# Kernel tuning notes

Measured on AMD Instinct MI355X. Metric: run time of the kernel, lower is better.

The kernel has to match this reference:

```python
import jax, jax.numpy as jnp
import numpy as np

B, S, HID = 2, 2048, 4096
H, KV, D = 32, 8, 128          # heads, kv heads, head_dim
G = H // KV                    # num_key_value_groups
THETA = 10000.0
SCALE = 1.0 / np.sqrt(D)
NEG_INF = -1e9


def rotate_half(x):
    x1, x2 = x[..., : D // 2], x[..., D // 2 :]
    return jnp.concatenate([-x2, x1], axis=-1)


def rope_tables(seq_len):
    inv_freq = 1.0 / (THETA ** (jnp.arange(0, D, 2, dtype=jnp.float32) / D))
    t = jnp.arange(seq_len, dtype=jnp.float32)
    freqs = jnp.outer(t, inv_freq)              # [S, D/2]
    emb = jnp.concatenate([freqs, freqs], -1)   # [S, D]
    return jnp.cos(emb), jnp.sin(emb)


def setup_inputs() -> dict:
    key = jax.random.key(0)
    ks = jax.random.split(key, 5)
    w = 0.02
    x = jax.random.normal(ks[0], (B, S, HID), jnp.float32)
    Wq = jax.random.normal(ks[1], (HID, H * D), jnp.float32) * w
    Wk = jax.random.normal(ks[2], (HID, KV * D), jnp.float32) * w
    Wv = jax.random.normal(ks[3], (HID, KV * D), jnp.float32) * w
    Wo = jax.random.normal(ks[4], (H * D, HID), jnp.float32) * w
    position_ids = jnp.broadcast_to(jnp.arange(S, dtype=jnp.int32), (B, S))
    causal = jnp.where(
        jnp.arange(S)[:, None] >= jnp.arange(S)[None, :], 0.0, NEG_INF
    ).astype(jnp.float32)
    attention_mask = jnp.broadcast_to(causal, (B, 1, S, S))
    return {
        "by_pass_hidden_states": x,
        "attention_mask": attention_mask,
        "position_ids": position_ids,
        "Wq": Wq,
        "Wk": Wk,
        "Wv": Wv,
        "Wo": Wo,
    }


def reference(by_pass_hidden_states, attention_mask, position_ids, Wq, Wk, Wv, Wo):
    x = by_pass_hidden_states
    # QKV projections (weights stored [in, out])
    q = (x @ Wq).reshape(B, S, H, D).transpose(0, 2, 1, 3)    # [B,H,S,D]
    k = (x @ Wk).reshape(B, S, KV, D).transpose(0, 2, 1, 3)   # [B,KV,S,D]
    v = (x @ Wv).reshape(B, S, KV, D).transpose(0, 2, 1, 3)   # [B,KV,S,D]
    # RoPE
    cos_t, sin_t = rope_tables(S)
    cos = cos_t[position_ids][:, None]   # [B,1,S,D]
    sin = sin_t[position_ids][:, None]
    q = q * cos + rotate_half(q) * sin
    k = k * cos + rotate_half(k) * sin
    # GQA attention without materializing repeated K/V: group query heads
    qg = q.reshape(B, KV, G, S, D)
    scores = jnp.einsum("bkgsd,bktd->bkgst", qg, k) * SCALE   # [B,KV,G,S,S]
    scores = scores.reshape(B, H, S, S) + attention_mask
    probs = jax.nn.softmax(scores.astype(jnp.float32), axis=-1).astype(x.dtype)
    ctx = jnp.einsum("bkgst,bktd->bkgsd", probs.reshape(B, KV, G, S, S), v)
    ctx = ctx.reshape(B, H, S, D).transpose(0, 2, 1, 3).reshape(B, S, H * D)
    return ctx @ Wo
```

## Files before the change

### kernel.cpp

```cpp
#include <hip/hip_runtime.h>
#include <cstdint>
#include <cstddef>

#define B_   2
#define S_   2048
#define HID_ 4096
#define H_   32
#define KV_  8
#define D_   128
#define M_   (B_*S_)
#define QSTR 6144

typedef __attribute__((ext_vector_type(8))) short bf16x8;
typedef __attribute__((ext_vector_type(4))) float f32x4;
typedef __attribute__((ext_vector_type(16))) float f32x16;
typedef __attribute__((ext_vector_type(4))) unsigned int u32x4;
typedef unsigned short u16;
typedef unsigned int   u32;

#define KSC (0.08838834764831845f * 1.4426950408889634f)

__device__ __forceinline__ float bf2f(u16 v){ u32 u = ((u32)v) << 16; return __builtin_bit_cast(float, u); }
__device__ __forceinline__ u16 f2bf(float f){
  u32 u = __builtin_bit_cast(u32, f);
  u32 r = u + 0x7fffu + ((u >> 16) & 1u);
  return (u16)(r >> 16);
}

__device__ __forceinline__ void gload_lds16(const void* g, void* lds){
  __builtin_amdgcn_global_load_lds(
      (const __attribute__((address_space(1))) void*)g,
      (__attribute__((address_space(3))) void*)lds, 16, 0, 0);
}

__global__ void cast_f32_bf16(const float* __restrict__ in, u16* __restrict__ out, int n){
  int i = (blockIdx.x * blockDim.x + threadIdx.x) * 4;
  if (i >= n) return;
  float4 v = *(const float4*)(in + i);
  ushort4 o;
  o.x = f2bf(v.x); o.y = f2bf(v.y); o.z = f2bf(v.z); o.w = f2bf(v.w);
  *(ushort4*)(out + i) = o;
}

__global__ __launch_bounds__(256) void tcast(const float* __restrict__ W, u16* __restrict__ WT,
                                             int Kd, int Nd){
  __shared__ __align__(16) u16 t[64][65];
  int k0 = blockIdx.x * 64, n0 = blockIdx.y * 64;
  int lx = threadIdx.x & 15, ly = threadIdx.x >> 4;
  #pragma unroll
  for (int rr = 0; rr < 4; ++rr){
    int r = rr * 16 + ly;
    float4 v = *(const float4*)(W + (size_t)(k0 + r) * Nd + n0 + lx * 4);
    t[lx*4+0][r] = f2bf(v.x);
    t[lx*4+1][r] = f2bf(v.y);
    t[lx*4+2][r] = f2bf(v.z);
    t[lx*4+3][r] = f2bf(v.w);
  }
  __syncthreads();
  #pragma unroll
  for (int rr = 0; rr < 4; ++rr){
    int r = rr * 16 + ly;
    ushort4 o;
    o.x = t[r][lx*4+0]; o.y = t[r][lx*4+1]; o.z = t[r][lx*4+2]; o.w = t[r][lx*4+3];
    *(ushort4*)(WT + (size_t)(n0 + r) * Kd + k0 + lx * 4) = o;
  }
}

__global__ __launch_bounds__(256) void vtrans(const u16* __restrict__ QKV, u16* __restrict__ Vt){
  __shared__ __align__(16) u16 t[64][65];
  int stile = blockIdx.x;
  int b = blockIdx.y >> 4, vt = blockIdx.y & 15;
  int s0 = stile * 64, c0 = vt * 64;
  int lx = threadIdx.x & 15, ly = threadIdx.x >> 4;
  #pragma unroll
  for (int rr = 0; rr < 4; ++rr){
    int r = rr * 16 + ly;
    ushort4 v = *(const ushort4*)(QKV + (size_t)(b*S_ + s0 + r) * QSTR + 5120 + c0 + lx*4);
    t[lx*4+0][r]=v.x; t[lx*4+1][r]=v.y; t[lx*4+2][r]=v.z; t[lx*4+3][r]=v.w;
  }
  __syncthreads();
  #pragma unroll
  for (int rr = 0; rr < 4; ++rr){
    int r = rr * 16 + ly;
    ushort4 o;
    o.x=t[r][lx*4+0]; o.y=t[r][lx*4+1]; o.z=t[r][lx*4+2]; o.w=t[r][lx*4+3];
    *(ushort4*)(Vt + (size_t)(b*1024 + c0 + r) * S_ + s0 + lx*4) = o;
  }
}

__global__ void rope_k(u16* __restrict__ X, const int* __restrict__ pos, int hshift, int stride){
  int idx = blockIdx.x * 256 + threadIdx.x;
  int i = idx & 63;
  int h = (idx >> 6) & ((1 << hshift) - 1);
  int t = idx >> (6 + hshift);
  u16* p0 = X + (size_t)t * stride + h * D_ + i;
  float x1 = bf2f(p0[0]), x2 = bf2f(p0[64]);
  float fpos = (float)pos[t];
  float invf = exp2f(-(float)(2 * i) * (13.287712379549449f / 128.0f));
  float f = fpos * invf;
  float sv = __sinf(f), cv = __cosf(f);
  p0[0]  = f2bf(x1 * cv - x2 * sv);
  p0[64] = f2bf(x2 * cv + x1 * sv);
}


#define BAR() __builtin_amdgcn_s_barrier()

#define STG_A(PB, HALF, KT) do{ \
  gload_lds16(Ag + off0 + (size_t)(HALF)*1048576 + (size_t)(KT)*128, \
              (char*)smem + (PB)*32768 + (HALF)*16384 + w*1024); \
  gload_lds16(Ag + off0 + 524288 + (size_t)(HALF)*1048576 + (size_t)(KT)*128, \
              (char*)smem + (PB)*32768 + (HALF)*16384 + 8192 + w*1024); }while(0)
#define STG_B(PB, HALF, KT) do{ \
  gload_lds16(Bg + off0 + (size_t)(HALF)*1048576 + (size_t)(KT)*128, \
              (char*)smem + 65536 + (PB)*32768 + (HALF)*16384 + w*1024); \
  gload_lds16(Bg + off0 + 524288 + (size_t)(HALF)*1048576 + (size_t)(KT)*128, \
              (char*)smem + 65536 + (PB)*32768 + (HALF)*16384 + 8192 + w*1024); }while(0)

#define RD_A(DST, PP, HALF) do{ \
  _Pragma("unroll") for (int ks = 0; ks < 2; ++ks) \
  _Pragma("unroll") for (int m = 0; m < 4; ++m) \
    DST[ks][m] = *(const bf16x8*)&smem[(PP)*16384 + (HALF)*8192 + aRowBase + m*1024 + csw[ks]]; }while(0)
#define RD_B(DST, PP, HALF) do{ \
  _Pragma("unroll") for (int ks = 0; ks < 2; ++ks) \
  _Pragma("unroll") for (int n = 0; n < 2; ++n) \
    DST[ks][n] = *(const bf16x8*)&smem[32768 + (PP)*16384 + (HALF)*8192 + bRowBase + n*1024 + csw[ks]]; }while(0)

template<int MO, int NO>
__device__ __forceinline__ void mfma_quad(f32x4 (&acc)[8][4],
                                          const bf16x8 (&af)[2][4], const bf16x8 (&bf)[2][2]){
  __builtin_amdgcn_s_setprio(1);
  #pragma unroll
  for (int ks = 0; ks < 2; ++ks)
    #pragma unroll
    for (int m = 0; m < 4; ++m)
      #pragma unroll
      for (int n = 0; n < 2; ++n)
        acc[MO+m][NO+n] = __builtin_amdgcn_mfma_f32_16x16x32_bf16(af[ks][m], bf[ks][n], acc[MO+m][NO+n], 0, 0, 0);
  __builtin_amdgcn_s_setprio(0);
}

template<bool OUTF32>
__global__ __launch_bounds__(512, 2) void gemm256(const u16* __restrict__ A, const u16* __restrict__ Bt,
                                                  void* __restrict__ C, int Nn, int mt){
  __shared__ __align__(16) u16 smem[65536];
  const int tid = threadIdx.x;
  const int l = tid & 63, w = tid >> 6;
  const int lr = l & 15, lk = l >> 4;
  const int wr = w >> 2, wc = w & 3;

  const int nwg = gridDim.x;
  const int sbid = ((int)blockIdx.x & 7) * (nwg >> 3) + ((int)blockIdx.x >> 3);
  const int bx = sbid % mt, by = sbid / mt;
  const size_t arow0 = (size_t)bx * 256;
  const size_t brow0 = (size_t)by * 256;
  const char* Ag = (const char*)(A + arow0 * 4096);
  const char* Bg = (const char*)(Bt + brow0 * 4096);

  const size_t off0 = (size_t)(w * 8 + (l >> 3)) * 8192 + (size_t)(((l & 7) ^ (l >> 3)) << 4);

  const int aRowBase = (wr*64 + lr) * 64;
  const int bRowBase = (wc*32 + lr) * 64;
  int csw[2];
  csw[0] = ((lk     ) ^ (lr & 7)) << 3;
  csw[1] = ((lk + 4) ^ (lr & 7)) << 3;

  f32x4 acc[8][4];
  #pragma unroll
  for (int i = 0; i < 8; ++i)
    #pragma unroll
    for (int j = 0; j < 4; ++j){ acc[i][j][0]=0.f; acc[i][j][1]=0.f; acc[i][j][2]=0.f; acc[i][j][3]=0.f; }

  STG_A(0, 0, 0); STG_B(0, 0, 0); STG_A(0, 1, 0); STG_B(0, 1, 0);
  STG_A(1, 0, 1); STG_B(1, 0, 1); STG_A(1, 1, 1); STG_B(1, 1, 1);
  asm volatile("s_waitcnt vmcnt(8)" ::: "memory");
  BAR();
  bf16x8 a0c[2][4], b0c[2][2], a1f[2][4], b1f[2][2];
  RD_A(a0c, 0, 0); RD_B(b0c, 0, 0);

  for (int t = 0; t < 64; ++t){
    const int P = t & 1;
    RD_A(a1f, P, 1);
    BAR();
    mfma_quad<0,0>(acc, a0c, b0c);
    BAR();
    if (t < 62){ STG_A(P, 0, t+2); STG_B(P, 0, t+2); }
    RD_B(b1f, P, 1);
    BAR();
    mfma_quad<4,0>(acc, a1f, b0c);
    BAR();
    if (t < 62){
      STG_A(P, 1, t+2);
      asm volatile("s_waitcnt vmcnt(6)" ::: "memory");
    } else if (t == 62){
      asm volatile("s_waitcnt vmcnt(0)" ::: "memory");
    }
    BAR();
    mfma_quad<4,2>(acc, a1f, b1f);
    BAR();
    if (t < 62){ STG_B(P, 1, t+2); }
    BAR();
    mfma_quad<0,2>(acc, a0c, b1f);
    if (t < 63){ RD_A(a0c, P^1, 0); RD_B(b0c, P^1, 0); }
    BAR();
  }

  #pragma unroll
  for (int mh = 0; mh < 2; ++mh)
    #pragma unroll
    for (int m = 0; m < 4; ++m)
      #pragma unroll
      for (int nh = 0; nh < 2; ++nh)
        #pragma unroll
        for (int n = 0; n < 2; ++n)
          #pragma unroll
          for (int j = 0; j < 4; ++j){
            size_t gr = arow0 + mh*128 + wr*64 + m*16 + lk*4 + j;
            size_t gc = brow0 + nh*128 + wc*32 + n*16 + lr;
            float v = acc[mh*4+m][nh*2+n][j];
            if (OUTF32) ((float*)C)[gr * Nn + gc] = v;
            else        ((u16*)C)[gr * Nn + gc] = f2bf(v);
          }
}

__global__ __launch_bounds__(512, 2) void attn_k(const u16* __restrict__ QKV,
                                                 const u16* __restrict__ Vtg,
                                                 u16* __restrict__ ctx){
  __shared__ __align__(16) u16 smem[32768];
  const int tid = threadIdx.x;
  const int l = tid & 63, w = tid >> 6;
  const int lane31 = l & 31, hi = l >> 5;
  const int hb = blockIdx.x;
  const int b = hb >> 5, h = hb & 31, kvh = h >> 2;
  const int qb = 7 - blockIdx.y;
  const int q0w = qb * 256 + w * 32;
  const int qg = q0w + lane31;

  const u16* Qp = QKV + (size_t)b * S_ * QSTR + (size_t)h * D_;
  const char* Kp = (const char*)(QKV + (size_t)b * S_ * QSTR + 4096 + (size_t)kvh * D_);
  const char* Vp = (const char*)(Vtg + ((size_t)b * 1024 + kvh * 128) * S_);

  bf16x8 qf[8];
  #pragma unroll
  for (int dt = 0; dt < 8; ++dt)
    qf[dt] = *(const bf16x8*)(Qp + (size_t)qg * QSTR + dt * 16 + hi * 8);

  const int krow0 = (2*w)*4 + (l >> 4), krow1 = krow0 + 4;
  const size_t koff0 = (size_t)krow0 * (QSTR*2) + (((l & 15) << 4) ^ ((krow0 & 7) << 4));
  const size_t koff1 = (size_t)krow1 * (QSTR*2) + (((l & 15) << 4) ^ ((krow1 & 7) << 4));
  const int vrow0 = (2*w)*8 + (l >> 3), vrow1 = vrow0 + 8;
  const size_t voff0 = (size_t)vrow0 * (S_*2) + (((l & 7) << 4) ^ ((vrow0 & 7) << 4));
  const size_t voff1 = (size_t)vrow1 * (S_*2) + (((l & 7) << 4) ^ ((vrow1 & 7) << 4));

  f32x16 acc[4];
  #pragma unroll
  for (int dt = 0; dt < 4; ++dt)
    #pragma unroll
    for (int i = 0; i < 16; ++i) acc[dt][i] = 0.f;
  float mrow = -3e38f, lsum = 0.f;

  const int nt = qb * 4 + 4;

  auto STAGE = [&](int t, int bufn){
    char* Kb = (char*)smem + bufn * 16384;
    char* Vb = (char*)smem + 32768 + bufn * 16384;
    size_t kb = (size_t)t * 64 * (QSTR*2);
    size_t vb = (size_t)t * 128;
    gload_lds16(Kp + kb + koff0, Kb + (2*w)*1024);
    gload_lds16(Kp + kb + koff1, Kb + (2*w+1)*1024);
    gload_lds16(Vp + vb + voff0, Vb + (2*w)*1024);
    gload_lds16(Vp + vb + voff1, Vb + (2*w+1)*1024);
  };

  STAGE(0, 0);
  __syncthreads();
  int buf = 0;
  for (int t = 0; t < nt; ++t){
    if (t + 1 < nt) STAGE(t + 1, buf ^ 1);
    const int kbase = t * 64;
    if (kbase <= q0w + 31){
      const char* Kb = (const char*)smem + buf * 16384;
      const char* Vb = (const char*)smem + 32768 + buf * 16384;
      const int swz = (lane31 & 7) << 4;

      f32x16 s0, s1;
      #pragma unroll
      for (int i = 0; i < 16; ++i){ s0[i] = 0.f; s1[i] = 0.f; }
      #pragma unroll
      for (int dt = 0; dt < 8; ++dt){
        bf16x8 kf = *(const bf16x8*)(Kb + lane31*256 + ((dt*32 + hi*16) ^ swz));
        s0 = __builtin_amdgcn_mfma_f32_32x32x16_bf16(kf, qf[dt], s0, 0, 0, 0);
      }
      #pragma unroll
      for (int dt = 0; dt < 8; ++dt){
        bf16x8 kf = *(const bf16x8*)(Kb + (32 + lane31)*256 + ((dt*32 + hi*16) ^ swz));
        s1 = __builtin_amdgcn_mfma_f32_32x32x16_bf16(kf, qf[dt], s1, 0, 0, 0);
      }

      if (kbase + 63 > q0w){
        int thr = qg - kbase;
        #pragma unroll
        for (int r = 0; r < 16; ++r){
          int kc = (r & 3) + 8*(r >> 2) + 4*hi;
          s0[r] = (kc > thr)      ? -1e30f : s0[r];
          s1[r] = (kc + 32 > thr) ? -1e30f : s1[r];
        }
      }

      float tmax = s0[0];
      #pragma unroll
      for (int r = 1; r < 16; ++r) tmax = fmaxf(tmax, s0[r]);
      #pragma unroll
      for (int r = 0; r < 16; ++r) tmax = fmaxf(tmax, s1[r]);
      tmax = fmaxf(tmax, __shfl_xor(tmax, 32));
      float mn = fmaxf(mrow, tmax);
      float rf = exp2f((mrow - mn) * KSC);
      mrow = mn;
      float ps = 0.f;
      #pragma unroll
      for (int r = 0; r < 16; ++r){
        float a = exp2f((s0[r] - mn) * KSC);
        float c = exp2f((s1[r] - mn) * KSC);
        s0[r] = a; s1[r] = c; ps += a + c;
      }
      ps += __shfl_xor(ps, 32);
      lsum = lsum * rf + ps;
      #pragma unroll
      for (int dt = 0; dt < 4; ++dt)
        #pragma unroll
        for (int i = 0; i < 16; ++i) acc[dt][i] *= rf;

      u32 pw[16];
      #pragma unroll
      for (int g = 0; g < 4; ++g){
        pw[2*g]     = (u32)f2bf(s0[4*g])   | ((u32)f2bf(s0[4*g+1]) << 16);
        pw[2*g+1]   = (u32)f2bf(s0[4*g+2]) | ((u32)f2bf(s0[4*g+3]) << 16);
        pw[8+2*g]   = (u32)f2bf(s1[4*g])   | ((u32)f2bf(s1[4*g+1]) << 16);
        pw[8+2*g+1] = (u32)f2bf(s1[4*g+2]) | ((u32)f2bf(s1[4*g+3]) << 16);
      }

      #pragma unroll
      for (int kt = 0; kt < 4; ++kt){
        u32 W0 = pw[kt*4+0], W1 = pw[kt*4+1], W2 = pw[kt*4+2], W3 = pw[kt*4+3];
        u32 x0 = hi ? W0 : W2;
        u32 x1 = hi ? W1 : W3;
        u32 y0 = __shfl_xor(x0, 32);
        u32 y1 = __shfl_xor(x1, 32);
        u32 w0 = hi ? y0 : W0;
        u32 w1 = hi ? y1 : W1;
        u32 w2 = hi ? W2 : y0;
        u32 w3 = hi ? W3 : y1;
        u32x4 pk; pk[0]=w0; pk[1]=w1; pk[2]=w2; pk[3]=w3;
        bf16x8 pa = __builtin_bit_cast(bf16x8, pk);
        #pragma unroll
        for (int dt = 0; dt < 4; ++dt){
          bf16x8 vf = *(const bf16x8*)(Vb + (dt*32 + lane31)*128 + ((kt*32 + hi*16) ^ swz));
          acc[dt] = __builtin_amdgcn_mfma_f32_32x32x16_bf16(vf, pa, acc[dt], 0, 0, 0);
        }
      }
    }
    __syncthreads();
    buf ^= 1;
  }

  __syncthreads();
  u16* Ot = smem + w * 4096;
  float inv = 1.f / lsum;
  #pragma unroll
  for (int dt = 0; dt < 4; ++dt)
    #pragma unroll
    for (int r = 0; r < 16; ++r){
      int d = dt*32 + (r & 3) + 8*(r >> 2) + 4*hi;
      Ot[lane31*128 + (d ^ ((lane31 & 15) << 2))] = f2bf(acc[dt][r] * inv);
    }
  u16* outp = ctx + ((size_t)(b * S_ + q0w)) * HID_ + h * D_;
  #pragma unroll
  for (int it = 0; it < 16; ++it){
    int id = it * 64 + l;
    int q = id >> 5;
    int c4 = (id & 31) * 4;
    ushort4 vv = *(const ushort4*)(Ot + q*128 + (c4 ^ ((q & 15) << 2)));
    *(ushort4*)(outp + (size_t)q * HID_ + c4) = vv;
  }
}

extern "C" void kernel_launch(void* const* d_in, const int* in_sizes, int n_in,
                              void* d_out, int out_size, void* d_ws, size_t ws_size,
                              hipStream_t stream) {
  const float* x  = (const float*)d_in[0];
  const int*   pos = (const int*)d_in[2];
  const float* Wq = (const float*)d_in[3];
  const float* Wk = (const float*)d_in[4];
  const float* Wv = (const float*)d_in[5];
  const float* Wo = (const float*)d_in[6];

  char* ws = (char*)d_ws;
  u16* xb   = (u16*)(ws);
  u16* WT   = (u16*)(ws + ((size_t)32 << 20));
  u16* WoT  = (u16*)(ws + ((size_t)80 << 20));
  u16* QKVb = (u16*)(ws + ((size_t)112 << 20));
  u16* Vtg  = (u16*)(ws + ((size_t)32 << 20));

  cast_f32_bf16<<<16384, 256, 0, stream>>>(x, xb, HID_ * M_);
  tcast<<<dim3(64, 64), 256, 0, stream>>>(Wq, WT, 4096, 4096);
  tcast<<<dim3(64, 16), 256, 0, stream>>>(Wk, WT + (size_t)4096 * 4096, 4096, 1024);
  tcast<<<dim3(64, 16), 256, 0, stream>>>(Wv, WT + (size_t)5120 * 4096, 4096, 1024);
  tcast<<<dim3(64, 64), 256, 0, stream>>>(Wo, WoT, 4096, 4096);
  gemm256<false><<<16 * 24, 512, 0, stream>>>(xb, WT, QKVb, 6144, 16);
  rope_k<<<32768, 256, 0, stream>>>(QKVb,        pos, 5, QSTR);
  rope_k<<<8192,  256, 0, stream>>>(QKVb + 4096, pos, 3, QSTR);
  vtrans<<<dim3(32, 32), 256, 0, stream>>>(QKVb, Vtg);
  attn_k<<<dim3(64, 8), 512, 0, stream>>>(QKVb, Vtg, xb);
  gemm256<true><<<16 * 16, 512, 0, stream>>>(xb, WoT, d_out, 4096, 16);
}
```

Measured before the change: 542.1 us.

## Use 256x192 tile GEMM for QKV projection to fill all CUs

Adds a gemm192 kernel with 256x192 output tiles and swaps it in for the QKV projection, which goes from a 384-block grid of 256x256 tiles to 512 blocks. The aim is to remove the wave-quantization tail on a 256-CU device, where 384 blocks leave the second round half empty. The new kernel has its own LDS staging and MFMA interleave for the 3-fragment-wide B tile, which adds code complexity. It also rereads A across more column tiles.

```diff
diff --git a/kernel.cpp b/kernel.cpp
--- a/kernel.cpp
+++ b/kernel.cpp
@@ -103,7 +103,6 @@
   p0[64] = f2bf(x2 * cv + x1 * sv);
 }
 
-
 #define BAR() __builtin_amdgcn_s_barrier()
 
 #define STG_A(PB, HALF, KT) do{ \
@@ -221,6 +220,127 @@
             if (OUTF32) ((float*)C)[gr * Nn + gc] = v;
             else        ((u16*)C)[gr * Nn + gc] = f2bf(v);
           }
+}
+
+#define STG_B3(PB, KT) do{ \
+  _Pragma("unroll") for (int r2 = 0; r2 < 3; ++r2) \
+    gload_lds16(Bg + bsrc3[r2] + (size_t)(KT)*128, \
+                (char*)smem + 65536 + (PB)*24576 + r2*8192 + w*1024); }while(0)
+
+#define RD_B0(DST, PP) do{ \
+  _Pragma("unroll") for (int ks = 0; ks < 2; ++ks) \
+  _Pragma("unroll") for (int n = 0; n < 2; ++n) \
+    DST[ks][n] = *(const bf16x8*)&smem[32768 + (PP)*12288 + bRowBase + n*1024 + csw[ks]]; }while(0)
+#define RD_B1(DST, PP) do{ \
+  _Pragma("unroll") for (int ks = 0; ks < 2; ++ks) \
+    DST[ks] = *(const bf16x8*)&smem[32768 + (PP)*12288 + bRowBase + 2048 + csw[ks]]; }while(0)
+
+__device__ __forceinline__ void mfma_pair16(f32x4 (&acc)[8][3], int MO,
+                                            const bf16x8 (&af)[2][4], const bf16x8 (&bf)[2][2]){
+  __builtin_amdgcn_s_setprio(1);
+  #pragma unroll
+  for (int ks = 0; ks < 2; ++ks)
+    #pragma unroll
+    for (int m = 0; m < 4; ++m)
+      #pragma unroll
+      for (int n = 0; n < 2; ++n)
+        acc[MO+m][n] = __builtin_amdgcn_mfma_f32_16x16x32_bf16(af[ks][m], bf[ks][n], acc[MO+m][n], 0, 0, 0);
+  __builtin_amdgcn_s_setprio(0);
+}
+__device__ __forceinline__ void mfma_pair8(f32x4 (&acc)[8][3], int MO,
+                                           const bf16x8 (&af)[2][4], const bf16x8 (&bf)[2]){
+  __builtin_amdgcn_s_setprio(1);
+  #pragma unroll
+  for (int ks = 0; ks < 2; ++ks)
+    #pragma unroll
+    for (int m = 0; m < 4; ++m)
+      acc[MO+m][2] = __builtin_amdgcn_mfma_f32_16x16x32_bf16(af[ks][m], bf[ks], acc[MO+m][2], 0, 0, 0);
+  __builtin_amdgcn_s_setprio(0);
+}
+
+__global__ __launch_bounds__(512, 2) void gemm192(const u16* __restrict__ A, const u16* __restrict__ Bt,
+                                                  u16* __restrict__ C, int Nn, int mt){
+  __shared__ __align__(16) u16 smem[57344];
+  const int tid = threadIdx.x;
+  const int l = tid & 63, w = tid >> 6;
+  const int lr = l & 15, lk = l >> 4;
+  const int wr = w >> 2, wc = w & 3;
+
+  const int nwg = gridDim.x;
+  const int sbid = ((int)blockIdx.x & 7) * (nwg >> 3) + ((int)blockIdx.x >> 3);
+  const int bx = sbid % mt, by = sbid / mt;
+  const size_t arow0 = (size_t)bx * 256;
+  const size_t bcol0 = (size_t)by * 192;
+  const char* Ag = (const char*)(A + arow0 * 4096);
+  const char* Bg = (const char*)(Bt + bcol0 * 4096);
+
+  const size_t off0 = (size_t)(w * 8 + (l >> 3)) * 8192 + (size_t)(((l & 7) ^ (l >> 3)) << 4);
+  size_t bsrc3[3];
+  #pragma unroll
+  for (int r2 = 0; r2 < 3; ++r2){
+    int idx = r2 * 512 + tid;
+    int row = idx >> 3, ch = idx & 7;
+    bsrc3[r2] = (size_t)row * 8192 + (size_t)((ch ^ (row & 7)) << 4);
+  }
+
+  const int aRowBase = (wr*64 + lr) * 64;
+  const int bRowBase = (wc*48 + lr) * 64;
+  int csw[2];
+  csw[0] = ((lk     ) ^ (lr & 7)) << 3;
+  csw[1] = ((lk + 4) ^ (lr & 7)) << 3;
+
+  f32x4 acc[8][3];
+  #pragma unroll
+  for (int i = 0; i < 8; ++i)
+    #pragma unroll
+    for (int j = 0; j < 3; ++j){ acc[i][j][0]=0.f; acc[i][j][1]=0.f; acc[i][j][2]=0.f; acc[i][j][3]=0.f; }
+
+  STG_A(0, 0, 0); STG_A(0, 1, 0); STG_B3(0, 0);
+  STG_A(1, 0, 1); STG_A(1, 1, 1); STG_B3(1, 1);
+  asm volatile("s_waitcnt vmcnt(7)" ::: "memory");
+  BAR();
+  bf16x8 a0c[2][4], a1f[2][4], b0c[2][2], b1f[2];
+  RD_A(a0c, 0, 0); RD_B0(b0c, 0);
+
+  for (int t = 0; t < 64; ++t){
+    const int P = t & 1;
+    RD_A(a1f, P, 1);
+    BAR();
+    mfma_pair16(acc, 0, a0c, b0c);
+    BAR();
+    if (t < 62){ STG_A(P, 0, t+2); }
+    RD_B1(b1f, P);
+    BAR();
+    mfma_pair16(acc, 4, a1f, b0c);
+    BAR();
+    if (t < 62){
+      STG_A(P, 1, t+2);
+      asm volatile("s_waitcnt vmcnt(4)" ::: "memory");
+    } else if (t == 62){
+      asm volatile("s_waitcnt vmcnt(0)" ::: "memory");
+    }
+    BAR();
+    mfma_pair8(acc, 4, a1f, b1f);
+    BAR();
+    if (t < 62){ STG_B3(P, t+2); }
+    BAR();
+    mfma_pair8(acc, 0, a0c, b1f);
+    if (t < 63){ RD_A(a0c, P^1, 0); RD_B0(b0c, P^1); }
+    BAR();
+  }
+
+  #pragma unroll
+  for (int mh = 0; mh < 2; ++mh)
+    #pragma unroll
+    for (int m = 0; m < 4; ++m)
+      #pragma unroll
+      for (int f = 0; f < 3; ++f)
+        #pragma unroll
+        for (int j = 0; j < 4; ++j){
+          size_t gr = arow0 + mh*128 + wr*64 + m*16 + lk*4 + j;
+          size_t gc = bcol0 + wc*48 + f*16 + lr;
+          C[gr * Nn + gc] = f2bf(acc[mh*4+m][f][j]);
+        }
 }
 
 __global__ __launch_bounds__(512, 2) void attn_k(const u16* __restrict__ QKV,
@@ -406,10 +526,10 @@
   tcast<<<dim3(64, 16), 256, 0, stream>>>(Wk, WT + (size_t)4096 * 4096, 4096, 1024);
   tcast<<<dim3(64, 16), 256, 0, stream>>>(Wv, WT + (size_t)5120 * 4096, 4096, 1024);
   tcast<<<dim3(64, 64), 256, 0, stream>>>(Wo, WoT, 4096, 4096);
-  gemm256<false><<<16 * 24, 512, 0, stream>>>(xb, WT, QKVb, 6144, 16);
+  gemm192<<<512, 512, 0, stream>>>(xb, WT, QKVb, 6144, 16);
   rope_k<<<32768, 256, 0, stream>>>(QKVb,        pos, 5, QSTR);
   rope_k<<<8192,  256, 0, stream>>>(QKVb + 4096, pos, 3, QSTR);
   vtrans<<<dim3(32, 32), 256, 0, stream>>>(QKVb, Vtg);
   attn_k<<<dim3(64, 8), 512, 0, stream>>>(QKVb, Vtg, xb);
-  gemm256<true><<<16 * 16, 512, 0, stream>>>(xb, WoT, d_out, 4096, 16);
-}
+  gemm256<true><<<256, 512, 0, stream>>>(xb, WoT, d_out, 4096, 16);
+}
```

After: 517.2 us. 4.6% less time.
